# Kernel optimization log

Measured on AMD Instinct MI355X. Metric: run time of the kernel, lower is better.

## Reference

```python
import jax, jax.numpy as jnp
import numpy as np

ALPHA = 0.2  # LeakyReLU negative slope (init arg alpha)


def setup_inputs() -> dict:
    key = jax.random.key(0)
    k1, k2, k3 = jax.random.split(key, 3)
    B, N, F_in, F_out = 8, 2048, 256, 256
    inp = jax.random.normal(k1, (B, N, F_in), dtype=jnp.float32)
    adj = jnp.ones((B, N, N), dtype=jnp.float32)  # unused by the module's forward
    # xavier_uniform with gain=1.414
    gain = 1.414
    bW = gain * np.sqrt(6.0 / (F_in + F_out))
    W = jax.random.uniform(k2, (F_in, F_out), minval=-bW, maxval=bW, dtype=jnp.float32)
    ba = gain * np.sqrt(6.0 / (2 * F_out + 1))
    a = jax.random.uniform(k3, (2 * F_out, 1), minval=-ba, maxval=ba, dtype=jnp.float32)
    return {"inp": inp, "adj": adj, "W": W, "a": a}


def reference(inp, adj, W, a):
    # inp: [B, N, F_in]; W: [F_in, F_out]; a: [2*F_out, 1]. adj is unused (as in source).
    F_out = W.shape[1]
    h = jnp.matmul(inp, W)  # [B, N, F_out]
    # e[b,i,j] = leakyrelu(a1 . h_i + a2 . h_j)  (equivalent to the repeat+cat+matmul)
    a1 = a[:F_out, 0]
    a2 = a[F_out:, 0]
    s1 = jnp.einsum('bnf,f->bn', h, a1)  # [B, N]
    s2 = jnp.einsum('bnf,f->bn', h, a2)  # [B, N]
    e = jax.nn.leaky_relu(s1[:, :, None] + s2[:, None, :], negative_slope=ALPHA)  # [B, N, N]
    # global per-batch min-max normalization, then affine *30 - 20
    mn = jnp.min(e, axis=(1, 2), keepdims=True)
    mx = jnp.max(e, axis=(1, 2), keepdims=True)
    e = (e - mn) / (mx - mn) * 30.0 - 20.0
    attention = jax.nn.sigmoid(e)  # dropout p=0 / eval: identity
    h_prime = jnp.matmul(attention, h)  # [B, N, F_out]
    h_prime = jax.nn.elu(h_prime)  # concat=True branch
    return h_prime, attention
```

## Files before the change

### kernel.cpp

```cpp
#include <hip/hip_runtime.h>
#include <stdint.h>

#define B_   8
#define N_   2048
#define F_   256
#define BN_  (B_ * N_)
#define ALPHA_ 0.2f

typedef __attribute__((ext_vector_type(8))) short  short8;
typedef __attribute__((ext_vector_type(4))) float  f32x4;

__device__ __forceinline__ unsigned short f2bf(float x) {
  uint32_t u = __float_as_uint(x);
  uint32_t r = (u + 0x7fffu + ((u >> 16) & 1u)) >> 16;
  return (unsigned short)r;
}

__device__ __forceinline__ uint32_t fkey(float f) {
  uint32_t b = __float_as_uint(f);
  return b ^ (uint32_t)(((int32_t)b >> 31) | (int32_t)0x80000000);
}
__device__ __forceinline__ float ikey(uint32_t k) {
  uint32_t b = (k & 0x80000000u) ? (k ^ 0x80000000u) : ~k;
  return __uint_as_float(b);
}

__device__ __forceinline__ void nt_store4(float* p, f32x4 v) {
  __builtin_nontemporal_store(v, (f32x4*)p);
}


__global__ void k_cvt_w(const float* __restrict__ W, unsigned short* __restrict__ WT2,
                        uint32_t* __restrict__ maxk, uint32_t* __restrict__ mink) {
  int k = blockIdx.x, n = threadIdx.x;
  if (k == 0 && n < 16) { maxk[n] = 0u; mink[n] = 0xFFFFFFFFu; }
  int idx = (((n >> 4) * 8 + (k >> 5)) << 9)
          + ((((k >> 3) & 3) << 4) + (n & 15)) * 8
          + (k & 7);
  WT2[idx] = f2bf(W[k * F_ + n]);
}

__launch_bounds__(256, 2)
__global__ void k_gemm1(const float* __restrict__ inp,
                        const unsigned short* __restrict__ WT2,
                        const float* __restrict__ avec,
                        unsigned short* __restrict__ hT2,
                        float* __restrict__ s1g, float* __restrict__ s2g,
                        uint32_t* __restrict__ maxk, uint32_t* __restrict__ mink) {
  __shared__ __align__(16) unsigned short Atile[64 * 32];
  __shared__ __align__(16) unsigned short Trans[256 * 72];
  __shared__ float s1_lds[64], s2_lds[64];

  const int tid  = threadIdx.x;
  const int wave = tid >> 6, lane = tid & 63;
  const int n16  = lane & 15, quad = lane >> 4;
  const int i0   = blockIdx.x * 64;
  const int b    = i0 >> 11;

  if (tid < 64) { s1_lds[tid] = 0.0f; s2_lds[tid] = 0.0f; }

  f32x4 acc[4][4];
  #pragma unroll
  for (int mt = 0; mt < 4; ++mt)
    #pragma unroll
    for (int nt = 0; nt < 4; ++nt) acc[mt][nt] = (f32x4){0.f, 0.f, 0.f, 0.f};

  const unsigned short* wbase = WT2 + (size_t)(wave * 32) * 512 + lane * 8;

  short8 bfA[4], bfB[4];
  #pragma unroll
  for (int nt = 0; nt < 4; ++nt)
    bfA[nt] = *(const short8*)(wbase + (nt * 8 + 0) * 512);

  auto body = [&](int t, short8* bfc, short8* bfn) {
    const int k0 = t << 5;
    {
      int r = tid >> 2, cp = tid & 3;
      const float* gp = inp + (size_t)(i0 + r) * F_ + k0 + cp * 8;
      float4 va = *(const float4*)gp;
      float4 vb = *(const float4*)(gp + 4);
      short8 sv;
      sv[0] = (short)f2bf(va.x); sv[1] = (short)f2bf(va.y);
      sv[2] = (short)f2bf(va.z); sv[3] = (short)f2bf(va.w);
      sv[4] = (short)f2bf(vb.x); sv[5] = (short)f2bf(vb.y);
      sv[6] = (short)f2bf(vb.z); sv[7] = (short)f2bf(vb.w);
      *(short8*)((char*)Atile + r * 64 + cp * 16) = sv;
    }
    __syncthreads();

    short8 af[4];
    #pragma unroll
    for (int mt = 0; mt < 4; ++mt)
      af[mt] = *(const short8*)((const char*)Atile + ((mt * 16 + n16) * 64 + quad * 16));

    if (t < 7) {
      #pragma unroll
      for (int nt = 0; nt < 4; ++nt)
        bfn[nt] = *(const short8*)(wbase + (nt * 8 + t + 1) * 512);
    }

    #pragma unroll
    for (int mt = 0; mt < 4; ++mt)
      #pragma unroll
      for (int nt = 0; nt < 4; ++nt)
        acc[mt][nt] = __builtin_amdgcn_mfma_f32_16x16x32_bf16(af[mt], bfc[nt], acc[mt][nt], 0, 0, 0);
    __syncthreads();
  };

  #pragma unroll
  for (int tt = 0; tt < 8; tt += 2) {
    body(tt, bfA, bfB);
    body(tt + 1, bfB, bfA);
  }

  #pragma unroll
  for (int mt = 0; mt < 4; ++mt)
    #pragma unroll
    for (int nt = 0; nt < 4; ++nt) {
      int f = (wave << 6) + (nt << 4) + n16;
      int i = (mt << 4) + (quad << 2);
      ushort4 pk;
      pk.x = f2bf(acc[mt][nt][0]); pk.y = f2bf(acc[mt][nt][1]);
      pk.z = f2bf(acc[mt][nt][2]); pk.w = f2bf(acc[mt][nt][3]);
      *(ushort4*)(Trans + f * 72 + i) = pk;
    }

  float a1v[4], a2v[4];
  #pragma unroll
  for (int nt = 0; nt < 4; ++nt) {
    int f = (wave << 6) + (nt << 4) + n16;
    a1v[nt] = avec[f];
    a2v[nt] = avec[F_ + f];
  }
  #pragma unroll
  for (int mt = 0; mt < 4; ++mt) {
    float s1p[4] = {0, 0, 0, 0}, s2p[4] = {0, 0, 0, 0};
    #pragma unroll
    for (int nt = 0; nt < 4; ++nt)
      #pragma unroll
      for (int rg = 0; rg < 4; ++rg) {
        s1p[rg] = fmaf(acc[mt][nt][rg], a1v[nt], s1p[rg]);
        s2p[rg] = fmaf(acc[mt][nt][rg], a2v[nt], s2p[rg]);
      }
    #pragma unroll
    for (int rg = 0; rg < 4; ++rg) {
      float v1 = s1p[rg], v2 = s2p[rg];
      #pragma unroll
      for (int off = 1; off < 16; off <<= 1) {
        v1 += __shfl_xor(v1, off);
        v2 += __shfl_xor(v2, off);
      }
      if (n16 == 0) {
        atomicAdd(&s1_lds[(mt << 4) + (quad << 2) + rg], v1);
        atomicAdd(&s2_lds[(mt << 4) + (quad << 2) + rg], v2);
      }
    }
  }
  __syncthreads();

  const int kb0 = (i0 & 2047) >> 5;
  #pragma unroll
  for (int p = 0; p < 8; ++p) {
    int f0  = p * 2 + (wave >> 1);
    int kbl = wave & 1;
    short8 v = *(const short8*)(Trans + (16 * f0 + (lane & 15)) * 72 + kbl * 32 + (lane >> 4) * 8);
    *(short8*)(hT2 + (size_t)((b * 16 + f0) * 64 + kb0 + kbl) * 512 + lane * 8) = v;
  }

  if (tid < 64) {
    float v1 = s1_lds[tid], v2 = s2_lds[tid];
    s1g[i0 + tid] = v1;
    s2g[i0 + tid] = v2;
    float mn1 = v1, mx1 = v1, mn2 = v2, mx2 = v2;
    #pragma unroll
    for (int off = 1; off < 64; off <<= 1) {
      mn1 = fminf(mn1, __shfl_xor(mn1, off));
      mx1 = fmaxf(mx1, __shfl_xor(mx1, off));
      mn2 = fminf(mn2, __shfl_xor(mn2, off));
      mx2 = fmaxf(mx2, __shfl_xor(mx2, off));
    }
    if (tid == 0) {
      atomicMax(&maxk[b * 2 + 0], fkey(mx1));
      atomicMax(&maxk[b * 2 + 1], fkey(mx2));
      atomicMin(&mink[b * 2 + 0], fkey(mn1));
      atomicMin(&mink[b * 2 + 1], fkey(mn2));
    }
  }
}

__launch_bounds__(256, 2)
__global__ void k_gemm2(const unsigned short* __restrict__ hT2,
                        const float* __restrict__ s1, const float* __restrict__ s2,
                        const uint32_t* __restrict__ maxk, const uint32_t* __restrict__ mink,
                        float* __restrict__ hprime,
                        float* __restrict__ att) {
  const int tid  = threadIdx.x;
  const int wave = tid >> 6, lane = tid & 63;
  const int n16  = lane & 15, quad = lane >> 4;
  const int wm   = wave >> 1, wn = wave & 1;
  const int blk  = blockIdx.x;
  const int b    = blk & 7;
  const int i0   = (blk >> 3) * 32;

  float mx1 = ikey(maxk[b * 2 + 0]), mx2 = ikey(maxk[b * 2 + 1]);
  float mn1 = ikey(mink[b * 2 + 0]), mn2 = ikey(mink[b * 2 + 1]);
  float smn = mn1 + mn2, smx = mx1 + mx2;
  float emn = fmaxf(smn, ALPHA_ * smn);
  float emx = fmaxf(smx, ALPHA_ * smx);
  float scale  = 30.0f / (emx - emn);
  const float uscale = -scale;
  const float ubias  = emn * scale + 20.0f;

  const int   myrow = 16 * wm + n16;
  const float s1v   = s1[b * N_ + i0 + myrow];
  const float* s2q  = s2 + b * N_ + quad * 8;
  float* attrow = att + ((size_t)(b * N_ + i0 + myrow)) * N_;

  const unsigned short* hbase = hT2 + (size_t)((b * 16 + 8 * wn) * 64) * 512 + lane * 8;

  f32x4 acc[8];
  #pragma unroll
  for (int nt = 0; nt < 8; ++nt) acc[nt] = (f32x4){0.f, 0.f, 0.f, 0.f};

  short8 bfA[8], bfB[8];
  float4 vaA, vbA, vaB, vbB;
  #pragma unroll
  for (int nt = 0; nt < 8; ++nt)
    bfA[nt] = *(const short8*)(hbase + (size_t)(nt * 64) * 512);
  vaA = *(const float4*)(s2q);
  vbA = *(const float4*)(s2q + 4);

  auto body = [&](int t, short8* bfc, float4& vac, float4& vbc,
                  short8* bfn, float4& van, float4& vbn) {
    const int k0 = t << 5;

    if (t < 63) {
      #pragma unroll
      for (int nt = 0; nt < 8; ++nt)
        bfn[nt] = *(const short8*)(hbase + (size_t)(nt * 64 + t + 1) * 512);
      van = *(const float4*)(s2q + k0 + 32);
      vbn = *(const float4*)(s2q + k0 + 36);
    }

    float v[8] = {vac.x, vac.y, vac.z, vac.w, vbc.x, vbc.y, vbc.z, vbc.w};
    #pragma unroll
    for (int jj = 0; jj < 8; ++jj) {
      float s = s1v + v[jj];
      float l = fmaxf(s, ALPHA_ * s);
      float u = fmaf(l, uscale, ubias);
      v[jj] = __builtin_amdgcn_rcpf(1.0f + __expf(u));
    }
    if (wn == 0) {
      *(f32x4*)(attrow + k0 + quad * 8)     = (f32x4){v[0], v[1], v[2], v[3]};
      *(f32x4*)(attrow + k0 + quad * 8 + 4) = (f32x4){v[4], v[5], v[6], v[7]};
    }

    short8 af;
    af[0] = (short)f2bf(v[0]); af[1] = (short)f2bf(v[1]);
    af[2] = (short)f2bf(v[2]); af[3] = (short)f2bf(v[3]);
    af[4] = (short)f2bf(v[4]); af[5] = (short)f2bf(v[5]);
    af[6] = (short)f2bf(v[6]); af[7] = (short)f2bf(v[7]);

    #pragma unroll
    for (int nt = 0; nt < 8; ++nt)
      acc[nt] = __builtin_amdgcn_mfma_f32_16x16x32_bf16(af, bfc[nt], acc[nt], 0, 0, 0);
  };

  for (int tt = 0; tt < 64; tt += 2) {
    body(tt,     bfA, vaA, vbA, bfB, vaB, vbB);
    body(tt + 1, bfB, vaB, vbB, bfA, vaA, vbA);
  }

  float* hp = hprime + ((size_t)(b * N_ + i0)) * F_;
  #pragma unroll
  for (int nt = 0; nt < 8; ++nt) {
    int fcol = 128 * wn + nt * 16 + n16;
    int irow = 16 * wm + quad * 4;
    #pragma unroll
    for (int rg = 0; rg < 4; ++rg) {
      float x = acc[nt][rg];
      float y = x > 0.0f ? x : (__expf(x) - 1.0f);
      __builtin_nontemporal_store(y, hp + (size_t)(irow + rg) * F_ + fcol);
    }
  }
}

extern "C" void kernel_launch(void* const* d_in, const int* in_sizes, int n_in,
                              void* d_out, int out_size, void* d_ws, size_t ws_size,
                              hipStream_t stream) {
  const float* inp  = (const float*)d_in[0];
  const float* W    = (const float*)d_in[2];
  const float* avec = (const float*)d_in[3];

  float* hprime = (float*)d_out;
  float* att    = (float*)d_out + (size_t)B_ * N_ * F_;

  char* ws = (char*)d_ws;
  unsigned short* WT2 = (unsigned short*)ws;
  unsigned short* hT2 = (unsigned short*)(ws + 131072);
  float* s1           = (float*)(ws + 131072 + 8388608);
  float* s2           = s1 + BN_;
  uint32_t* maxk      = (uint32_t*)(s2 + BN_);
  uint32_t* mink      = maxk + 16;

  k_cvt_w<<<F_, F_, 0, stream>>>(W, WT2, maxk, mink);
  k_gemm1<<<BN_ / 64, 256, 0, stream>>>(inp, WT2, avec, hT2, s1, s2, maxk, mink);
  k_gemm2<<<512, 256, 0, stream>>>(hT2, s1, s2, maxk, mink, hprime, att);
}
```

Before: 283.3 us.

## Stage h tiles and s2 through LDS with async double-buffered loads in gemm2

Rewrites the attention-times-h kernel so that h tiles are copied into double-buffered shared memory with global_load_lds async loads and s2 is preloaded into LDS once per block. Each attention value is computed exactly once per block and shared with all waves through an LDS A-tile. Before, the two waves covering different feature halves each recomputed the sigmoid for the same rows. The wave layout changes from a 2x2 split to each wave owning 64 feature columns across all 32 rows. The cost is a block-wide barrier every k-step and higher LDS use (about 44 KB), which may limit occupancy.

```diff
diff --git a/kernel.cpp b/kernel.cpp
--- a/kernel.cpp
+++ b/kernel.cpp
@@ -25,8 +25,10 @@
   return __uint_as_float(b);
 }
 
-__device__ __forceinline__ void nt_store4(float* p, f32x4 v) {
-  __builtin_nontemporal_store(v, (f32x4*)p);
+__device__ __forceinline__ void async_load16(const void* g, void* l) {
+  __builtin_amdgcn_global_load_lds(
+      (const __attribute__((address_space(1))) uint32_t*)g,
+      (__attribute__((address_space(3))) uint32_t*)l, 16, 0, 0);
 }
 
 
@@ -194,10 +196,13 @@
                         const uint32_t* __restrict__ maxk, const uint32_t* __restrict__ mink,
                         float* __restrict__ hprime,
                         float* __restrict__ att) {
+  __shared__ __align__(16) char Btile[2][16384];
+  __shared__ __align__(16) unsigned short Atile[2][1024];
+  __shared__ __align__(16) float s2_lds[N_];
+
   const int tid  = threadIdx.x;
   const int wave = tid >> 6, lane = tid & 63;
   const int n16  = lane & 15, quad = lane >> 4;
-  const int wm   = wave >> 1, wn = wave & 1;
   const int blk  = blockIdx.x;
   const int b    = blk & 7;
   const int i0   = (blk >> 3) * 32;
@@ -211,78 +216,90 @@
   const float uscale = -scale;
   const float ubias  = emn * scale + 20.0f;
 
-  const int   myrow = 16 * wm + n16;
-  const float s1v   = s1[b * N_ + i0 + myrow];
-  const float* s2q  = s2 + b * N_ + quad * 8;
-  float* attrow = att + ((size_t)(b * N_ + i0 + myrow)) * N_;
-
-  const unsigned short* hbase = hT2 + (size_t)((b * 16 + 8 * wn) * 64) * 512 + lane * 8;
-
-  f32x4 acc[8];
-  #pragma unroll
-  for (int nt = 0; nt < 8; ++nt) acc[nt] = (f32x4){0.f, 0.f, 0.f, 0.f};
-
-  short8 bfA[8], bfB[8];
-  float4 vaA, vbA, vaB, vbB;
-  #pragma unroll
-  for (int nt = 0; nt < 8; ++nt)
-    bfA[nt] = *(const short8*)(hbase + (size_t)(nt * 64) * 512);
-  vaA = *(const float4*)(s2q);
-  vbA = *(const float4*)(s2q + 4);
-
-  auto body = [&](int t, short8* bfc, float4& vac, float4& vbc,
-                  short8* bfn, float4& van, float4& vbn) {
-    const int k0 = t << 5;
-
-    if (t < 63) {
-      #pragma unroll
-      for (int nt = 0; nt < 8; ++nt)
-        bfn[nt] = *(const short8*)(hbase + (size_t)(nt * 64 + t + 1) * 512);
-      van = *(const float4*)(s2q + k0 + 32);
-      vbn = *(const float4*)(s2q + k0 + 36);
-    }
-
-    float v[8] = {vac.x, vac.y, vac.z, vac.w, vbc.x, vbc.y, vbc.z, vbc.w};
-    #pragma unroll
-    for (int jj = 0; jj < 8; ++jj) {
+  const int r_att = tid >> 3;
+  const int c_att = tid & 7;
+  const float s1v = s1[b * N_ + i0 + r_att];
+  const float* s2b = s2 + b * N_;
+  float* attrow = att + ((size_t)(b * N_ + i0 + r_att)) * N_;
+
+  auto stage_b = [&](int buf_, int kb) {
+    #pragma unroll
+    for (int g = 0; g < 4; ++g) {
+      int f0 = wave * 4 + g;
+      async_load16(hT2 + ((size_t)((b * 16 + f0) * 64 + kb) << 9) + lane * 8,
+                   (char*)Btile + buf_ * 16384 + (f0 << 10));
+    }
+  };
+
+  #pragma unroll
+  for (int it = 0; it < 2; ++it)
+    async_load16(s2b + wave * 512 + it * 256 + lane * 4,
+                 (char*)s2_lds + wave * 2048 + it * 1024);
+  stage_b(0, 0);
+  asm volatile("s_waitcnt vmcnt(0) lgkmcnt(0)" ::: "memory");
+  __builtin_amdgcn_s_barrier();
+  asm volatile("" ::: "memory");
+
+  f32x4 acc[2][4];
+  #pragma unroll
+  for (int mt = 0; mt < 2; ++mt)
+    #pragma unroll
+    for (int nt = 0; nt < 4; ++nt) acc[mt][nt] = (f32x4){0.f, 0.f, 0.f, 0.f};
+
+  for (int t = 0; t < 64; ++t) {
+    const int cur  = t & 1;
+    const int abuf = cur * 2048;
+    const int k0   = t << 5;
+
+    float4 va = *(const float4*)((const char*)s2_lds + k0 * 4 + c_att * 16);
+    float v[4] = {va.x, va.y, va.z, va.w};
+    #pragma unroll
+    for (int jj = 0; jj < 4; ++jj) {
       float s = s1v + v[jj];
       float l = fmaxf(s, ALPHA_ * s);
       float u = fmaf(l, uscale, ubias);
       v[jj] = __builtin_amdgcn_rcpf(1.0f + __expf(u));
     }
-    if (wn == 0) {
-      *(f32x4*)(attrow + k0 + quad * 8)     = (f32x4){v[0], v[1], v[2], v[3]};
-      *(f32x4*)(attrow + k0 + quad * 8 + 4) = (f32x4){v[4], v[5], v[6], v[7]};
-    }
-
-    short8 af;
-    af[0] = (short)f2bf(v[0]); af[1] = (short)f2bf(v[1]);
-    af[2] = (short)f2bf(v[2]); af[3] = (short)f2bf(v[3]);
-    af[4] = (short)f2bf(v[4]); af[5] = (short)f2bf(v[5]);
-    af[6] = (short)f2bf(v[6]); af[7] = (short)f2bf(v[7]);
-
-    #pragma unroll
-    for (int nt = 0; nt < 8; ++nt)
-      acc[nt] = __builtin_amdgcn_mfma_f32_16x16x32_bf16(af, bfc[nt], acc[nt], 0, 0, 0);
-  };
-
-  for (int tt = 0; tt < 64; tt += 2) {
-    body(tt,     bfA, vaA, vbA, bfB, vaB, vbB);
-    body(tt + 1, bfB, vaB, vbB, bfA, vaA, vbA);
+    *(f32x4*)(attrow + k0 + c_att * 4) = (f32x4){v[0], v[1], v[2], v[3]};
+    ushort4 spk;
+    spk.x = f2bf(v[0]); spk.y = f2bf(v[1]); spk.z = f2bf(v[2]); spk.w = f2bf(v[3]);
+    *(ushort4*)((char*)Atile + abuf + tid * 8) = spk;
+
+    asm volatile("s_waitcnt vmcnt(1) lgkmcnt(0)" ::: "memory");
+    __builtin_amdgcn_s_barrier();
+    asm volatile("" ::: "memory");
+
+    if (t < 63) stage_b(cur ^ 1, t + 1);
+
+    short8 af0 = *(const short8*)((const char*)Atile + abuf + n16 * 64 + quad * 16);
+    short8 af1 = *(const short8*)((const char*)Atile + abuf + (16 + n16) * 64 + quad * 16);
+    short8 bf_[4];
+    #pragma unroll
+    for (int nt = 0; nt < 4; ++nt)
+      bf_[nt] = *(const short8*)((const char*)Btile + cur * 16384 +
+                                 ((wave * 4 + nt) << 10) + lane * 16);
+
+    #pragma unroll
+    for (int nt = 0; nt < 4; ++nt) {
+      acc[0][nt] = __builtin_amdgcn_mfma_f32_16x16x32_bf16(af0, bf_[nt], acc[0][nt], 0, 0, 0);
+      acc[1][nt] = __builtin_amdgcn_mfma_f32_16x16x32_bf16(af1, bf_[nt], acc[1][nt], 0, 0, 0);
+    }
   }
 
   float* hp = hprime + ((size_t)(b * N_ + i0)) * F_;
   #pragma unroll
-  for (int nt = 0; nt < 8; ++nt) {
-    int fcol = 128 * wn + nt * 16 + n16;
-    int irow = 16 * wm + quad * 4;
-    #pragma unroll
-    for (int rg = 0; rg < 4; ++rg) {
-      float x = acc[nt][rg];
-      float y = x > 0.0f ? x : (__expf(x) - 1.0f);
-      __builtin_nontemporal_store(y, hp + (size_t)(irow + rg) * F_ + fcol);
-    }
-  }
+  for (int mt = 0; mt < 2; ++mt)
+    #pragma unroll
+    for (int nt = 0; nt < 4; ++nt) {
+      int fcol = (wave << 6) + (nt << 4) + n16;
+      int irow = (mt << 4) + (quad << 2);
+      #pragma unroll
+      for (int rg = 0; rg < 4; ++rg) {
+        float x = acc[mt][nt][rg];
+        float y = x > 0.0f ? x : (__expf(x) - 1.0f);
+        __builtin_nontemporal_store(y, hp + (size_t)(irow + rg) * F_ + fcol);
+      }
+    }
 }
 
 extern "C" void kernel_launch(void* const* d_in, const int* in_sizes, int n_in,
```

After: 282.8 us. About the same (-0.2%).
